# Kernel tuning notes

Hardware: AMD Instinct MI355X
Metric: run time of the kernel (lower is better)

## Reference

```python
import jax, jax.numpy as jnp
import numpy as np

SCALE = 0.08838834764831845  # 1/sqrt(head_size=128)
NEG_INF = -1e9


def setup_inputs() -> dict:
    key = jax.random.key(0)
    ks = jax.random.split(key, 8)
    NH, HS = 32, 128                 # heads, head_size
    NP, NS, G = 2048, 4, 64          # prompt tokens, prompt seqs, decode tokens
    NT = NP + G                      # total valid tokens
    NB, BS, MB = 1024, 16, 32        # num cache blocks, block_size, max blocks/seq
    q = jax.random.normal(ks[0], (NT, NH * HS), jnp.float32)
    k = jax.random.normal(ks[1], (NT, NH * HS), jnp.float32)
    v = jax.random.normal(ks[2], (NT, NH * HS), jnp.float32)
    kc = jax.random.normal(ks[3], (NB, NH, HS, BS), jnp.float32)
    vc = jax.random.normal(ks[4], (NB, NH, HS, BS), jnp.float32)
    bt = jax.random.randint(ks[5], (G, MB), 0, NB, jnp.int32)
    cl = jax.random.randint(ks[6], (G,), 1, MB * BS + 1, jnp.int32)  # >=1 so softmax is defined
    sm = jax.random.randint(ks[7], (NT,), 0, NB * BS, jnp.int32)
    return {"query": q, "key": k, "value": v, "key_cache": kc, "value_cache": vc,
            "block_tables": bt, "context_lens": cl, "slot_mapping": sm,
            "num_prompt_tokens": NP, "num_prompt_seqs": NS}


def reference(query, key, value, key_cache, value_cache, block_tables,
              context_lens, slot_mapping, num_prompt_tokens, num_prompt_seqs):
    NB, NH, HS, BS = key_cache.shape
    q = query.reshape(-1, NH, HS)
    k = key.reshape(-1, NH, HS)
    v = value.reshape(-1, NH, HS)
    NP, NS = num_prompt_tokens, num_prompt_seqs
    L = NP // NS  # equal-length prompts -> block-diagonal causal == batched causal

    # --- prompt phase: multi-query causal MHA (xformers path) ---
    qp = q[:NP].reshape(NS, L, NH, HS)
    kp = k[:NP].reshape(NS, L, NH, HS)
    vp = v[:NP].reshape(NS, L, NH, HS)
    scores = jnp.einsum('bqhd,bkhd->bhqk', qp, kp) * SCALE
    causal = jnp.tril(jnp.ones((L, L), bool))
    scores = jnp.where(causal, scores, NEG_INF)
    probs = jax.nn.softmax(scores, axis=-1)
    out_p = jnp.einsum('bhqk,bkhd->bqhd', probs, vp).reshape(NP, NH, HS)

    # --- reshape_and_cache: scatter all valid tokens' K/V into paged cache ---
    blk = slot_mapping // BS
    off = slot_mapping % BS
    key_cache = key_cache.at[blk, :, :, off].set(k)
    value_cache = value_cache.at[blk, :, :, off].set(v)

    # --- decode phase: single-query paged attention over block tables ---
    qd = q[NP:]                                  # [G, NH, HS]
    G, MB = block_tables.shape
    # gather blocks: [G, MB, NH, HS, BS] -> [G, MB*BS, NH, HS]
    kd = jnp.transpose(key_cache[block_tables], (0, 1, 4, 2, 3)).reshape(G, MB * BS, NH, HS)
    vd = jnp.transpose(value_cache[block_tables], (0, 1, 4, 2, 3)).reshape(G, MB * BS, NH, HS)
    sc = jnp.einsum('ghd,gkhd->ghk', qd, kd) * SCALE
    valid = jnp.arange(MB * BS)[None, :] < context_lens[:, None]   # [G, K]
    sc = jnp.where(valid[:, None, :], sc, NEG_INF)
    pd = jax.nn.softmax(sc, axis=-1)
    out_d = jnp.einsum('ghk,gkhd->ghd', pd, vd)

    out = jnp.concatenate([out_p, out_d], axis=0)
    return out.reshape(-1, NH * HS)
```

## Files before the change

kernel.cpp:

```cpp
#include <hip/hip_runtime.h>
#include <stdint.h>

#define NH    32
#define HS    128
#define NPT   2048
#define NT    2112
#define NBLK  1024
#define BS    16
#define MBMAX 32
#define LSEQ  512
#define DMODEL 4096
#define SCALE 0.08838834764831845f

typedef __bf16 bf16x8 __attribute__((ext_vector_type(8)));
typedef float  f32x4  __attribute__((ext_vector_type(4)));

__device__ __forceinline__ unsigned short f2bf(float f) {
    unsigned u = __float_as_uint(f);
    u += 0x7fffu + ((u >> 16) & 1u);
    return (unsigned short)(u >> 16);
}
__device__ __forceinline__ unsigned pack2(float a, float b) {
    return (unsigned)f2bf(a) | ((unsigned)f2bf(b) << 16);
}
__device__ __forceinline__ float sel4(const float a[4], int i) {
    float r = a[0];
    r = (i == 1) ? a[1] : r;
    r = (i == 2) ? a[2] : r;
    r = (i == 3) ? a[3] : r;
    return r;
}

__global__ void init_winner(int* __restrict__ w) {
    int i = blockIdx.x * 256 + threadIdx.x;
    if (i < NBLK * BS) w[i] = -1;
}
__global__ void fill_winner(const int* __restrict__ sm, int* __restrict__ w) {
    int t = blockIdx.x * 256 + threadIdx.x;
    if (t < NT) atomicMax(&w[sm[t]], t);
}

#define QKS 136
__device__ __forceinline__ int vtidx(int d, int t) {
    return d * 72 + (t ^ (((d >> 3) & 3) * 8));
}

__global__ __launch_bounds__(256, 2) void prompt_attn(
    const float* __restrict__ q, const float* __restrict__ k,
    const float* __restrict__ v, float* __restrict__ out) {

    __shared__ __align__(16) unsigned short Qs[64 * QKS];
    __shared__ __align__(16) unsigned short Ks[64 * QKS];
    __shared__ __align__(16) unsigned short Vt[128 * 72 + 32];
    __shared__ __align__(16) unsigned short Ps[4 * 16 * 72];

    const int tid  = threadIdx.x;
    const int lane = tid & 63, wq = tid >> 6;
    const int quad = lane >> 4, m15 = lane & 15;
    const int qt = 7 - (blockIdx.x & 7);
    const int h  = (blockIdx.x >> 3) & 31;
    const int s  = blockIdx.x >> 8;
    const int qbase  = s * LSEQ + qt * 64;
    const int kbase0 = s * LSEQ;

    {
        const int r0 = tid >> 5, c4 = (tid & 31) * 4;
        #pragma unroll
        for (int p = 0; p < 8; ++p) {
            int r = r0 + p * 8;
            float4 t = *(const float4*)(q + (size_t)(qbase + r) * DMODEL + h * HS + c4);
            uint2 w; w.x = pack2(t.x * SCALE, t.y * SCALE); w.y = pack2(t.z * SCALE, t.w * SCALE);
            *(uint2*)(&Qs[r * QKS + c4]) = w;
        }
    }

    f32x4 O[8];
    #pragma unroll
    for (int i = 0; i < 8; ++i) O[i] = (f32x4){0.f, 0.f, 0.f, 0.f};
    float mrun[4], lrun[4];
    #pragma unroll
    for (int r = 0; r < 4; ++r) { mrun[r] = -1e30f; lrun[r] = 0.f; }

    unsigned short* Pw = Ps + wq * (16 * 72);

    for (int kt = 0; kt <= qt; ++kt) {
        {
            const int r0 = tid >> 5, c4 = (tid & 31) * 4;
            #pragma unroll
            for (int p = 0; p < 8; ++p) {
                int r = r0 + p * 8;
                float4 t = *(const float4*)(k + (size_t)(kbase0 + kt * 64 + r) * DMODEL + h * HS + c4);
                uint2 w; w.x = pack2(t.x, t.y); w.y = pack2(t.z, t.w);
                *(uint2*)(&Ks[r * QKS + c4]) = w;
            }
        }
        {
            const int g = tid >> 2, sub = tid & 3;
            const int lbase = lane & ~3;
            #pragma unroll
            for (int p = 0; p < 8; ++p) {
                const int tb = (p & 3) * 16, db = (p >> 2) * 64;
                const int tok  = tb + (g >> 4) * 4 + sub;
                const int dim4 = db + (g & 15) * 4;
                float4 t = *(const float4*)(v + (size_t)(kbase0 + kt * 64 + tok) * DMODEL + h * HS + dim4);
                float in[4] = {t.x, t.y, t.z, t.w};
                float rec[4];
                #pragma unroll
                for (int r = 0; r < 4; ++r) {
                    float pub = sel4(in, (sub + 4 - r) & 3);
                    rec[r] = __shfl(pub, lbase + ((sub + r) & 3));
                }
                float o4[4];
                #pragma unroll
                for (int j = 0; j < 4; ++j) o4[j] = sel4(rec, (j + 4 - sub) & 3);
                const int d  = dim4 + sub;
                const int t0 = tb + (g >> 4) * 4;
                uint2 w2; w2.x = pack2(o4[0], o4[1]); w2.y = pack2(o4[2], o4[3]);
                *(uint2*)(&Vt[vtidx(d, t0)]) = w2;
            }
        }
        __syncthreads();

        bf16x8 aq[4];
        #pragma unroll
        for (int kc = 0; kc < 4; ++kc)
            aq[kc] = *(const bf16x8*)(&Qs[(wq * 16 + m15) * QKS + kc * 32 + quad * 8]);
        f32x4 S[4];
        #pragma unroll
        for (int nt = 0; nt < 4; ++nt) {
            S[nt] = (f32x4){0.f, 0.f, 0.f, 0.f};
            #pragma unroll
            for (int kc = 0; kc < 4; ++kc) {
                bf16x8 bk = *(const bf16x8*)(&Ks[(nt * 16 + m15) * QKS + kc * 32 + quad * 8]);
                S[nt] = __builtin_amdgcn_mfma_f32_16x16x32_bf16(aq[kc], bk, S[nt], 0, 0, 0);
            }
        }
        if (kt == qt) {
            #pragma unroll
            for (int nt = 0; nt < 4; ++nt) {
                const int C = nt * 16 + m15;
                #pragma unroll
                for (int reg = 0; reg < 4; ++reg) {
                    const int R = wq * 16 + quad * 4 + reg;
                    if (C > R) S[nt][reg] = -1e30f;
                }
            }
        }

        #pragma unroll
        for (int reg = 0; reg < 4; ++reg) {
            float x = fmaxf(fmaxf(S[0][reg], S[1][reg]), fmaxf(S[2][reg], S[3][reg]));
            x = fmaxf(x, __shfl_xor(x, 1));
            x = fmaxf(x, __shfl_xor(x, 2));
            x = fmaxf(x, __shfl_xor(x, 4));
            x = fmaxf(x, __shfl_xor(x, 8));
            const float mn = fmaxf(mrun[reg], x);
            const float al = __expf(mrun[reg] - mn);
            mrun[reg] = mn;
            float sum = 0.f;
            #pragma unroll
            for (int nt = 0; nt < 4; ++nt) {
                float pv = __expf(S[nt][reg] - mn);
                S[nt][reg] = pv;
                sum += pv;
            }
            sum += __shfl_xor(sum, 1);
            sum += __shfl_xor(sum, 2);
            sum += __shfl_xor(sum, 4);
            sum += __shfl_xor(sum, 8);
            lrun[reg] = lrun[reg] * al + sum;
            #pragma unroll
            for (int n2 = 0; n2 < 8; ++n2) O[n2][reg] *= al;
        }

        #pragma unroll
        for (int nt = 0; nt < 4; ++nt) {
            #pragma unroll
            for (int reg = 0; reg < 4; ++reg) {
                float v0 = S[nt][reg];
                float v1 = __shfl_xor(v0, 1);
                if (!(lane & 1))
                    *(unsigned*)(&Pw[(quad * 4 + reg) * 72 + nt * 16 + m15]) = pack2(v0, v1);
            }
        }

        bf16x8 ap[2];
        #pragma unroll
        for (int kc = 0; kc < 2; ++kc)
            ap[kc] = *(const bf16x8*)(&Pw[m15 * 72 + kc * 32 + quad * 8]);
        #pragma unroll
        for (int n2 = 0; n2 < 8; ++n2) {
            #pragma unroll
            for (int kc = 0; kc < 2; ++kc) {
                bf16x8 bv = *(const bf16x8*)(&Vt[vtidx(n2 * 16 + m15, kc * 32 + quad * 8)]);
                O[n2] = __builtin_amdgcn_mfma_f32_16x16x32_bf16(ap[kc], bv, O[n2], 0, 0, 0);
            }
        }
        __syncthreads();
    }

    float inv[4];
    #pragma unroll
    for (int reg = 0; reg < 4; ++reg) inv[reg] = 1.f / lrun[reg];
    #pragma unroll
    for (int n2 = 0; n2 < 8; ++n2) {
        #pragma unroll
        for (int reg = 0; reg < 4; ++reg) {
            out[(size_t)(qbase + wq * 16 + quad * 4 + reg) * DMODEL + h * HS + n2 * 16 + m15] =
                O[n2][reg] * inv[reg];
        }
    }
}

__global__ __launch_bounds__(256, 4) void decode_attn(
    const float* __restrict__ q, const float* __restrict__ k, const float* __restrict__ v,
    const float* __restrict__ kcache, const float* __restrict__ vcache,
    const int* __restrict__ bt, const int* __restrict__ cl,
    const int* __restrict__ winner, float* __restrict__ out) {

    __shared__ float qs[128];
    __shared__ float tile[4][128 * 17];
    __shared__ float pm[4], pl[4];
    __shared__ float pacc[4][128];

    const int tid = threadIdx.x, w = tid >> 6, lane = tid & 63;
    const int g = blockIdx.x >> 5, h = blockIdx.x & 31;
    const int n  = cl[g];
    const int nb = (n + 15) >> 4;

    if (tid < 64) {
        const float2 t = *(const float2*)(q + (size_t)(NPT + g) * DMODEL + h * HS + tid * 2);
        qs[tid * 2] = t.x; qs[tid * 2 + 1] = t.y;
    }
    __syncthreads();

    const int c = lane >> 4, off = lane & 15;
    float qreg[32];
    #pragma unroll
    for (int i = 0; i < 32; ++i) qreg[i] = qs[i * 4 + c];

    float m = -1e30f, l = 0.f, a0 = 0.f, a1 = 0.f;
    float* T = tile[w];

    for (int jb = w; jb < nb; jb += 4) {
        const int blk = bt[g * MBMAX + jb];
        const int wt  = winner[blk * BS + off];
        const float* kb = kcache + ((size_t)blk * NH + h) * (HS * BS);

        #pragma unroll
        for (int i = 0; i < 8; ++i) {
            const int e = lane * 4 + i * 256;
            const float4 t = *(const float4*)(kb + e);
            const int d = e >> 4, of = e & 15;
            float* p = T + d * 17 + of;
            p[0] = t.x; p[1] = t.y; p[2] = t.z; p[3] = t.w;
        }
        #pragma unroll
        for (int o2 = 0; o2 < 16; ++o2) {
            const int wt2 = __shfl(wt, o2);
            if (wt2 >= 0) {
                const float* kr = k + (size_t)wt2 * DMODEL + h * HS;
                T[lane * 17 + o2]        = kr[lane];
                T[(lane + 64) * 17 + o2] = kr[lane + 64];
            }
        }
        float partial = 0.f;
        #pragma unroll
        for (int i = 0; i < 32; ++i) partial += qreg[i] * T[(i * 4 + c) * 17 + off];
        partial += __shfl_xor(partial, 16);
        partial += __shfl_xor(partial, 32);
        float sv = partial * SCALE;
        if (jb * 16 + off >= n) sv = -1e30f;

        float tm = sv;
        tm = fmaxf(tm, __shfl_xor(tm, 1));
        tm = fmaxf(tm, __shfl_xor(tm, 2));
        tm = fmaxf(tm, __shfl_xor(tm, 4));
        tm = fmaxf(tm, __shfl_xor(tm, 8));
        const float mn = fmaxf(m, tm);
        const float al = __expf(m - mn);
        const float p  = __expf(sv - mn);
        float ps = p;
        ps += __shfl_xor(ps, 1);
        ps += __shfl_xor(ps, 2);
        ps += __shfl_xor(ps, 4);
        ps += __shfl_xor(ps, 8);
        l = l * al + ps;
        m = mn;
        a0 *= al; a1 *= al;

        const float* vb = vcache + ((size_t)blk * NH + h) * (HS * BS);
        #pragma unroll
        for (int i = 0; i < 8; ++i) {
            const int e = lane * 4 + i * 256;
            const float4 t = *(const float4*)(vb + e);
            const int d = e >> 4, of = e & 15;
            float* pp = T + d * 17 + of;
            pp[0] = t.x; pp[1] = t.y; pp[2] = t.z; pp[3] = t.w;
        }
        #pragma unroll
        for (int o2 = 0; o2 < 16; ++o2) {
            const int wt2 = __shfl(wt, o2);
            if (wt2 >= 0) {
                const float* vr = v + (size_t)wt2 * DMODEL + h * HS;
                T[lane * 17 + o2]        = vr[lane];
                T[(lane + 64) * 17 + o2] = vr[lane + 64];
            }
        }
        #pragma unroll
        for (int o2 = 0; o2 < 16; ++o2) {
            const float pp = __shfl(p, o2);
            a0 += pp * T[lane * 17 + o2];
            a1 += pp * T[(lane + 64) * 17 + o2];
        }
    }

    if (lane == 0) { pm[w] = m; pl[w] = l; }
    pacc[w][lane]      = a0;
    pacc[w][lane + 64] = a1;
    __syncthreads();
    if (tid < 128) {
        const float M = fmaxf(fmaxf(pm[0], pm[1]), fmaxf(pm[2], pm[3]));
        float L = 0.f, A = 0.f;
        #pragma unroll
        for (int w2 = 0; w2 < 4; ++w2) {
            const float e = __expf(pm[w2] - M);
            L += e * pl[w2];
            A += e * pacc[w2][tid];
        }
        out[(size_t)(NPT + g) * DMODEL + h * HS + tid] = A / L;
    }
}

extern "C" void kernel_launch(void* const* d_in, const int* in_sizes, int n_in,
                              void* d_out, int out_size, void* d_ws, size_t ws_size,
                              hipStream_t stream) {
    const float* q  = (const float*)d_in[0];
    const float* k  = (const float*)d_in[1];
    const float* v  = (const float*)d_in[2];
    const float* kc = (const float*)d_in[3];
    const float* vc = (const float*)d_in[4];
    const int* bt   = (const int*)d_in[5];
    const int* cl   = (const int*)d_in[6];
    const int* sm   = (const int*)d_in[7];
    float* out  = (float*)d_out;
    int* winner = (int*)d_ws;

    hipLaunchKernelGGL(init_winner, dim3(64),   dim3(256), 0, stream, winner);
    hipLaunchKernelGGL(fill_winner, dim3(9),    dim3(256), 0, stream, sm, winner);
    hipLaunchKernelGGL(prompt_attn, dim3(1024), dim3(256), 0, stream, q, k, v, out);
    hipLaunchKernelGGL(decode_attn, dim3(2048), dim3(256), 0, stream,
                       q, k, v, kc, vc, bt, cl, winner, out);
}
```

Measured before the change: 755.8 us.

## Rewrite decode attention to keep K/V in registers and prefetch next block

The decode kernel no longer stages K/V blocks through a padded LDS tile. Each lane loads float4 vectors of the cache block straight into registers and computes partial dot products over 4 token offsets, reducing them with cross-lane shuffles. The next K block is prefetched while the current block's V is being consumed, and freshly written token overrides are applied per lane only when any winner exists. This removes LDS traffic and barriers but raises register use, so launch bounds drop from 4 to 3 waves per SIMD.

```diff
diff --git a/kernel.cpp b/kernel.cpp
--- a/kernel.cpp
+++ b/kernel.cpp
@@ -212,14 +212,12 @@
     }
 }
 
-__global__ __launch_bounds__(256, 4) void decode_attn(
+__global__ __launch_bounds__(256, 3) void decode_attn(
     const float* __restrict__ q, const float* __restrict__ k, const float* __restrict__ v,
     const float* __restrict__ kcache, const float* __restrict__ vcache,
     const int* __restrict__ bt, const int* __restrict__ cl,
     const int* __restrict__ winner, float* __restrict__ out) {
 
-    __shared__ float qs[128];
-    __shared__ float tile[4][128 * 17];
     __shared__ float pm[4], pl[4];
     __shared__ float pacc[4][128];
 
@@ -228,96 +226,119 @@
     const int n  = cl[g];
     const int nb = (n + 15) >> 4;
 
-    if (tid < 64) {
-        const float2 t = *(const float2*)(q + (size_t)(NPT + g) * DMODEL + h * HS + tid * 2);
-        qs[tid * 2] = t.x; qs[tid * 2 + 1] = t.y;
-    }
-    __syncthreads();
-
-    const int c = lane >> 4, off = lane & 15;
-    float qreg[32];
-    #pragma unroll
-    for (int i = 0; i < 32; ++i) qreg[i] = qs[i * 4 + c];
-
-    float m = -1e30f, l = 0.f, a0 = 0.f, a1 = 0.f;
-    float* T = tile[w];
+    const int p4 = lane >> 2;
+    const int ob = (lane & 3) * 4;
+
+    const float* qp = q + (size_t)(NPT + g) * DMODEL + h * HS;
+    float qreg[8];
+    #pragma unroll
+    for (int i = 0; i < 8; ++i) qreg[i] = qp[p4 + 16 * i] * SCALE;
+
+    float m = -1e30f, l = 0.f;
+    float acc[8];
+    #pragma unroll
+    for (int i = 0; i < 8; ++i) acc[i] = 0.f;
+
+    f32x4 kv[8], vv[8];
+    int blk = 0;
+    if (w < nb) {
+        blk = bt[g * MBMAX + w];
+        const float* kb = kcache + ((size_t)blk * NH + h) * (HS * BS);
+        #pragma unroll
+        for (int i = 0; i < 8; ++i)
+            kv[i] = *(const f32x4*)(kb + lane * 4 + i * 256);
+    }
 
     for (int jb = w; jb < nb; jb += 4) {
-        const int blk = bt[g * MBMAX + jb];
-        const int wt  = winner[blk * BS + off];
-        const float* kb = kcache + ((size_t)blk * NH + h) * (HS * BS);
-
+        const float* vb = vcache + ((size_t)blk * NH + h) * (HS * BS);
+        #pragma unroll
+        for (int i = 0; i < 8; ++i)
+            vv[i] = *(const f32x4*)(vb + lane * 4 + i * 256);
+
+        const int4 wt4 = *(const int4*)(winner + blk * BS + ob);
+        const int wtj[4] = {wt4.x, wt4.y, wt4.z, wt4.w};
+        const bool anyw = __any(wt4.x >= 0 || wt4.y >= 0 || wt4.z >= 0 || wt4.w >= 0);
+
+        if (anyw) {
+            #pragma unroll
+            for (int j = 0; j < 4; ++j) {
+                if (wtj[j] >= 0) {
+                    const float* fr = k + (size_t)wtj[j] * DMODEL + h * HS + p4;
+                    #pragma unroll
+                    for (int i = 0; i < 8; ++i) kv[i][j] = fr[16 * i];
+                }
+            }
+        }
+
+        float s[4];
+        #pragma unroll
+        for (int j = 0; j < 4; ++j) s[j] = 0.f;
         #pragma unroll
         for (int i = 0; i < 8; ++i) {
-            const int e = lane * 4 + i * 256;
-            const float4 t = *(const float4*)(kb + e);
-            const int d = e >> 4, of = e & 15;
-            float* p = T + d * 17 + of;
-            p[0] = t.x; p[1] = t.y; p[2] = t.z; p[3] = t.w;
-        }
-        #pragma unroll
-        for (int o2 = 0; o2 < 16; ++o2) {
-            const int wt2 = __shfl(wt, o2);
-            if (wt2 >= 0) {
-                const float* kr = k + (size_t)wt2 * DMODEL + h * HS;
-                T[lane * 17 + o2]        = kr[lane];
-                T[(lane + 64) * 17 + o2] = kr[lane + 64];
-            }
-        }
-        float partial = 0.f;
-        #pragma unroll
-        for (int i = 0; i < 32; ++i) partial += qreg[i] * T[(i * 4 + c) * 17 + off];
-        partial += __shfl_xor(partial, 16);
-        partial += __shfl_xor(partial, 32);
-        float sv = partial * SCALE;
-        if (jb * 16 + off >= n) sv = -1e30f;
-
-        float tm = sv;
+            s[0] += qreg[i] * kv[i][0];
+            s[1] += qreg[i] * kv[i][1];
+            s[2] += qreg[i] * kv[i][2];
+            s[3] += qreg[i] * kv[i][3];
+        }
+        #pragma unroll
+        for (int j = 0; j < 4; ++j) {
+            s[j] += __shfl_xor(s[j], 4);
+            s[j] += __shfl_xor(s[j], 8);
+            s[j] += __shfl_xor(s[j], 16);
+            s[j] += __shfl_xor(s[j], 32);
+            if (jb * 16 + ob + j >= n) s[j] = -1e30f;
+        }
+
+        float tm = fmaxf(fmaxf(s[0], s[1]), fmaxf(s[2], s[3]));
         tm = fmaxf(tm, __shfl_xor(tm, 1));
         tm = fmaxf(tm, __shfl_xor(tm, 2));
-        tm = fmaxf(tm, __shfl_xor(tm, 4));
-        tm = fmaxf(tm, __shfl_xor(tm, 8));
         const float mn = fmaxf(m, tm);
         const float al = __expf(m - mn);
-        const float p  = __expf(sv - mn);
-        float ps = p;
+        m = mn;
+        float p[4], ps = 0.f;
+        #pragma unroll
+        for (int j = 0; j < 4; ++j) { p[j] = __expf(s[j] - mn); ps += p[j]; }
         ps += __shfl_xor(ps, 1);
         ps += __shfl_xor(ps, 2);
-        ps += __shfl_xor(ps, 4);
-        ps += __shfl_xor(ps, 8);
         l = l * al + ps;
-        m = mn;
-        a0 *= al; a1 *= al;
-
-        const float* vb = vcache + ((size_t)blk * NH + h) * (HS * BS);
-        #pragma unroll
-        for (int i = 0; i < 8; ++i) {
-            const int e = lane * 4 + i * 256;
-            const float4 t = *(const float4*)(vb + e);
-            const int d = e >> 4, of = e & 15;
-            float* pp = T + d * 17 + of;
-            pp[0] = t.x; pp[1] = t.y; pp[2] = t.z; pp[3] = t.w;
-        }
-        #pragma unroll
-        for (int o2 = 0; o2 < 16; ++o2) {
-            const int wt2 = __shfl(wt, o2);
-            if (wt2 >= 0) {
-                const float* vr = v + (size_t)wt2 * DMODEL + h * HS;
-                T[lane * 17 + o2]        = vr[lane];
-                T[(lane + 64) * 17 + o2] = vr[lane + 64];
-            }
-        }
-        #pragma unroll
-        for (int o2 = 0; o2 < 16; ++o2) {
-            const float pp = __shfl(p, o2);
-            a0 += pp * T[lane * 17 + o2];
-            a1 += pp * T[(lane + 64) * 17 + o2];
-        }
-    }
-
+        #pragma unroll
+        for (int i = 0; i < 8; ++i) acc[i] *= al;
+
+        const int jn = jb + 4;
+        if (jn < nb) {
+            blk = bt[g * MBMAX + jn];
+            const float* kb = kcache + ((size_t)blk * NH + h) * (HS * BS);
+            #pragma unroll
+            for (int i = 0; i < 8; ++i)
+                kv[i] = *(const f32x4*)(kb + lane * 4 + i * 256);
+        }
+
+        if (anyw) {
+            #pragma unroll
+            for (int j = 0; j < 4; ++j) {
+                if (wtj[j] >= 0) {
+                    const float* fr = v + (size_t)wtj[j] * DMODEL + h * HS + p4;
+                    #pragma unroll
+                    for (int i = 0; i < 8; ++i) vv[i][j] = fr[16 * i];
+                }
+            }
+        }
+        #pragma unroll
+        for (int i = 0; i < 8; ++i)
+            acc[i] += p[0] * vv[i][0] + p[1] * vv[i][1]
+                    + p[2] * vv[i][2] + p[3] * vv[i][3];
+    }
+
+    #pragma unroll
+    for (int i = 0; i < 8; ++i) {
+        acc[i] += __shfl_xor(acc[i], 1);
+        acc[i] += __shfl_xor(acc[i], 2);
+    }
     if (lane == 0) { pm[w] = m; pl[w] = l; }
-    pacc[w][lane]      = a0;
-    pacc[w][lane + 64] = a1;
+    if ((lane & 3) == 0) {
+        #pragma unroll
+        for (int i = 0; i < 8; ++i) pacc[w][p4 + 16 * i] = acc[i];
+    }
     __syncthreads();
     if (tid < 128) {
         const float M = fmaxf(fmaxf(pm[0], pm[1]), fmaxf(pm[2], pm[3]));
```

Result: faster. 694.7 us (-8.1%).
